# Kernel tuning notes

Measured on AMD Instinct MI355X. Metric: run time of the kernel, lower is better.

The kernel has to match this reference:

```python
import jax, jax.numpy as jnp
import numpy as np

EPS = 1e-5
N, K, CIN, COUT = 100000, 27, 64, 128


def sparse_conv(x, nbr, W):
    # x: [N, C]; nbr: [N, K] with sentinel index N meaning 'no neighbor'
    x_pad = jnp.concatenate([x, jnp.zeros((1, x.shape[1]), x.dtype)], axis=0)  # [N+1, C]
    g = x_pad[nbr]  # gather: [N, K, C]
    return jnp.einsum('nkc,kcd->nd', g, W)  # per-offset GEMM, scatter to output sites


def bn_relu(y, gamma, beta):
    # BatchNorm over active sites (training-mode batch statistics), then ReLU
    mu = y.mean(axis=0)
    var = y.var(axis=0)
    return jax.nn.relu((y - mu) * jax.lax.rsqrt(var + EPS) * gamma + beta)


def setup_inputs() -> dict:
    key = jax.random.key(0)
    ks = jax.random.split(key, 5)
    x = jax.random.normal(ks[0], (N, CIN), dtype=jnp.float32)
    # sentinel N indicates missing neighbor (maps to zero-padded row)
    nbr = jax.random.randint(ks[1], (N, K), 0, N + 1)
    W1 = jax.random.normal(ks[2], (K, CIN, COUT), dtype=jnp.float32) * (1.0 / np.sqrt(K * CIN))
    W2 = jax.random.normal(ks[3], (K, COUT, COUT), dtype=jnp.float32) * (1.0 / np.sqrt(K * COUT))
    W_skip = jax.random.normal(ks[4], (CIN, COUT), dtype=jnp.float32) * (1.0 / np.sqrt(CIN))
    return {
        'x': x, 'nbr': nbr,
        'W1': W1, 'gamma1': jnp.ones((COUT,), jnp.float32), 'beta1': jnp.zeros((COUT,), jnp.float32),
        'W2': W2, 'gamma2': jnp.ones((COUT,), jnp.float32), 'beta2': jnp.zeros((COUT,), jnp.float32),
        'W_skip': W_skip,
    }


def reference(x, nbr, W1, gamma1, beta1, W2, gamma2, beta2, W_skip):
    identity = x @ W_skip                      # 1x1 conv skip (same coords)
    h = bn_relu(sparse_conv(x, nbr, W1), gamma1, beta1)
    h = bn_relu(sparse_conv(h, nbr, W2), gamma2, beta2)
    return h + identity
```

## Files before the change

### kernel.cpp

```cpp
#include <hip/hip_runtime.h>
#include <hip/hip_bf16.h>

#define NSITES 100000
#define KOFFS 27
#define CIN 64
#define COUT 128

typedef unsigned short u16;
typedef __attribute__((ext_vector_type(8))) short s16x8;
typedef __attribute__((ext_vector_type(4))) float f32x4;

static __device__ __forceinline__ u16 f2bf(float f) {
    union { float f; unsigned u; } x; x.f = f;
    return (u16)((x.u + 0x7FFFu + ((x.u >> 16) & 1u)) >> 16);
}
static __device__ __forceinline__ float bf2f(u16 v) {
    union { unsigned u; float f; } x; x.u = ((unsigned)v) << 16;
    return x.f;
}

__global__ void prep_kernel(const float* __restrict__ W1, const float* __restrict__ W2,
                            const float* __restrict__ Wsk,
                            u16* __restrict__ W1t, u16* __restrict__ W2t,
                            u16* __restrict__ Wskt, float* __restrict__ zero_area) {
    int i = blockIdx.x * 256 + threadIdx.x;
    if (i < 27 * 64 * 128) {
        int k = i / 8192, r = i & 8191, d = r >> 6, c = r & 63;
        W1t[i] = f2bf(W1[k * 8192 + c * 128 + d]);
        return;
    }
    i -= 27 * 64 * 128;
    if (i < 27 * 128 * 128) {
        int k = i / 16384, r = i & 16383, d = r >> 7, c = r & 127;
        W2t[i] = f2bf(W2[k * 16384 + c * 128 + d]);
        return;
    }
    i -= 27 * 128 * 128;
    if (i < 8192) {
        int d = i >> 6, c = i & 63;
        Wskt[i] = f2bf(Wsk[c * 128 + d]);
        return;
    }
    i -= 8192;
    zero_area[i] = 0.0f;
}

__global__ void convert_x_kernel(const float* __restrict__ x, u16* __restrict__ xb) {
    long long e = ((long long)blockIdx.x * 256 + threadIdx.x) * 8;
    if (e >= (long long)(NSITES + 1) * CIN) return;
    s16x8 o;
    if (e < (long long)NSITES * CIN) {
        float4 v0 = *(const float4*)(x + e);
        float4 v1 = *(const float4*)(x + e + 4);
        o[0] = (short)f2bf(v0.x); o[1] = (short)f2bf(v0.y);
        o[2] = (short)f2bf(v0.z); o[3] = (short)f2bf(v0.w);
        o[4] = (short)f2bf(v1.x); o[5] = (short)f2bf(v1.y);
        o[6] = (short)f2bf(v1.z); o[7] = (short)f2bf(v1.w);
    } else {
#pragma unroll
        for (int j = 0; j < 8; ++j) o[j] = 0;
    }
    *(s16x8*)(xb + e) = o;
}

template <int CK, bool IDENT_FUSE, bool STATS>
__global__ __launch_bounds__(256, (CK == 64 ? 4 : 3)) void conv_kernel(
    const u16* __restrict__ xin, const int* __restrict__ nbr,
    const u16* __restrict__ Wt, u16* __restrict__ yout,
    float* __restrict__ psum, float* __restrict__ psq, int nk,
    const u16* __restrict__ Wskt, float* __restrict__ outid) {
    constexpr int STRIDE = CK + 8;
    constexpr int KSTEPS = CK / 32;
    constexpr int CPR = CK / 8;
    constexpr int RPP = 256 / CPR;
    constexpr int NPASS = 64 / RPP;
    __shared__ __align__(16) u16 a_tile[2][64 * STRIDE];
    __shared__ int nbr_tile[64 * KOFFS];

    const int tid = threadIdx.x;
    const int wave = tid >> 6;
    const int lane = tid & 63;
    const int m = lane & 15;
    const int q = lane >> 4;
    const int n0 = blockIdx.x * 64;
    const int wc = wave * 32;
    const int srow = tid / CPR;
    const int schunk = tid % CPR;

    for (int i = tid; i < 64 * KOFFS; i += 256) {
        int r = i / KOFFS;
        int kk = i - r * KOFFS;
        int row = n0 + r;
        nbr_tile[i] = (row < NSITES) ? nbr[row * KOFFS + kk] : NSITES;
    }
    __syncthreads();

    f32x4 acc[4][2];
#pragma unroll
    for (int rt = 0; rt < 4; ++rt)
#pragma unroll
        for (int ct = 0; ct < 2; ++ct)
#pragma unroll
            for (int r = 0; r < 4; ++r) acc[rt][ct][r] = 0.0f;

    s16x8 ag[NPASS];
#pragma unroll
    for (int p = 0; p < NPASS; ++p) {
        int r = p * RPP + srow;
        ag[p] = *(const s16x8*)(xin + (long long)nbr_tile[r * KOFFS] * CK + schunk * 8);
    }
#pragma unroll
    for (int p = 0; p < NPASS; ++p)
        *(s16x8*)(a_tile[0] + (p * RPP + srow) * STRIDE + schunk * 8) = ag[p];
    __syncthreads();

    for (int k = 0; k < nk; ++k) {
        const u16* abuf = a_tile[k & 1];
        u16* wbuf = a_tile[(k + 1) & 1];
        const bool more = (k + 1 < nk);

        if (more) {
#pragma unroll
            for (int p = 0; p < NPASS; ++p) {
                int r = p * RPP + srow;
                ag[p] = *(const s16x8*)(xin + (long long)nbr_tile[r * KOFFS + k + 1] * CK + schunk * 8);
            }
        }

        s16x8 bf[2][KSTEPS];
        const u16* wb = Wt + (long long)k * (COUT * CK);
#pragma unroll
        for (int ct = 0; ct < 2; ++ct)
#pragma unroll
            for (int ks = 0; ks < KSTEPS; ++ks)
                bf[ct][ks] = *(const s16x8*)(wb + (wc + ct * 16 + m) * CK + ks * 32 + q * 8);

#pragma unroll
        for (int ks = 0; ks < KSTEPS; ++ks) {
            s16x8 af[4];
#pragma unroll
            for (int rt = 0; rt < 4; ++rt)
                af[rt] = *(const s16x8*)(abuf + (rt * 16 + m) * STRIDE + ks * 32 + q * 8);
#pragma unroll
            for (int rt = 0; rt < 4; ++rt)
#pragma unroll
                for (int ct = 0; ct < 2; ++ct)
                    acc[rt][ct] = __builtin_amdgcn_mfma_f32_16x16x32_bf16(
                        af[rt], bf[ct][ks], acc[rt][ct], 0, 0, 0);
        }

        if (more) {
#pragma unroll
            for (int p = 0; p < NPASS; ++p)
                *(s16x8*)(wbuf + (p * RPP + srow) * STRIDE + schunk * 8) = ag[p];
        }
        __syncthreads();
    }

#pragma unroll
    for (int rt = 0; rt < 4; ++rt) {
        int rowb = n0 + rt * 16 + q * 4;
#pragma unroll
        for (int ct = 0; ct < 2; ++ct) {
            int col = wc + ct * 16 + m;
#pragma unroll
            for (int r = 0; r < 4; ++r) {
                int row = rowb + r;
                if (row < NSITES) yout[(long long)row * COUT + col] = f2bf(acc[rt][ct][r]);
            }
        }
    }

    if (STATS) {
#pragma unroll
        for (int ct = 0; ct < 2; ++ct) {
            float s = 0.f, ss = 0.f;
#pragma unroll
            for (int rt = 0; rt < 4; ++rt)
#pragma unroll
                for (int r = 0; r < 4; ++r) {
                    float v = acc[rt][ct][r];
                    s += v; ss += v * v;
                }
            s += __shfl_xor(s, 16); ss += __shfl_xor(ss, 16);
            s += __shfl_xor(s, 32); ss += __shfl_xor(ss, 32);
            if (q == 0) {
                int col = wc + ct * 16 + m;
                int slot = blockIdx.x & 63;
                atomicAdd(psum + slot * COUT + col, s);
                atomicAdd(psq + slot * COUT + col, ss);
            }
        }
    }

    if (IDENT_FUSE) {
#pragma unroll
        for (int rt = 0; rt < 4; ++rt)
#pragma unroll
            for (int ct = 0; ct < 2; ++ct)
#pragma unroll
                for (int r = 0; r < 4; ++r) acc[rt][ct][r] = 0.0f;
        s16x8 aid[NPASS];
#pragma unroll
        for (int p = 0; p < NPASS; ++p) {
            int row = n0 + p * RPP + srow;
            long long idx = (row < NSITES) ? row : NSITES;
            aid[p] = *(const s16x8*)(xin + idx * CK + schunk * 8);
        }
        s16x8 bfi[2][KSTEPS];
#pragma unroll
        for (int ct = 0; ct < 2; ++ct)
#pragma unroll
            for (int ks = 0; ks < KSTEPS; ++ks)
                bfi[ct][ks] = *(const s16x8*)(Wskt + (wc + ct * 16 + m) * CK + ks * 32 + q * 8);
#pragma unroll
        for (int p = 0; p < NPASS; ++p)
            *(s16x8*)(a_tile[0] + (p * RPP + srow) * STRIDE + schunk * 8) = aid[p];
        __syncthreads();
#pragma unroll
        for (int ks = 0; ks < KSTEPS; ++ks) {
            s16x8 af[4];
#pragma unroll
            for (int rt = 0; rt < 4; ++rt)
                af[rt] = *(const s16x8*)(a_tile[0] + (rt * 16 + m) * STRIDE + ks * 32 + q * 8);
#pragma unroll
            for (int rt = 0; rt < 4; ++rt)
#pragma unroll
                for (int ct = 0; ct < 2; ++ct)
                    acc[rt][ct] = __builtin_amdgcn_mfma_f32_16x16x32_bf16(
                        af[rt], bfi[ct][ks], acc[rt][ct], 0, 0, 0);
        }
#pragma unroll
        for (int rt = 0; rt < 4; ++rt) {
            int rowb = n0 + rt * 16 + q * 4;
#pragma unroll
            for (int ct = 0; ct < 2; ++ct) {
                int col = wc + ct * 16 + m;
#pragma unroll
                for (int r = 0; r < 4; ++r) {
                    int row = rowb + r;
                    if (row < NSITES) outid[(long long)row * COUT + col] = acc[rt][ct][r];
                }
            }
        }
    }
}

__global__ void bn_stats_kernel(const float* __restrict__ psum, const float* __restrict__ psq,
                                const float* __restrict__ gamma, const float* __restrict__ beta,
                                float* __restrict__ ab) {
    int col = threadIdx.x;
    float s = 0.f, ss = 0.f;
    for (int i = 0; i < 64; ++i) { s += psum[i * COUT + col]; ss += psq[i * COUT + col]; }
    const float inv_n = 1.0f / (float)NSITES;
    float mu = s * inv_n;
    float var = ss * inv_n - mu * mu;
    float rs = rsqrtf(var + 1e-5f);
    float a = gamma[col] * rs;
    ab[col] = a;
    ab[COUT + col] = beta[col] - mu * a;
}

__global__ void bn_apply_kernel(const u16* __restrict__ y, const float* __restrict__ ab,
                                u16* __restrict__ h) {
    long long e = ((long long)blockIdx.x * 256 + threadIdx.x) * 8;
    if (e >= (long long)(NSITES + 1) * COUT) return;
    s16x8 o;
    if (e < (long long)NSITES * COUT) {
        int cb = (int)(e & (COUT - 1));
        s16x8 v = *(const s16x8*)(y + e);
#pragma unroll
        for (int j = 0; j < 8; ++j) {
            float r = bf2f((u16)v[j]) * ab[cb + j] + ab[COUT + cb + j];
            o[j] = (short)f2bf(fmaxf(r, 0.f));
        }
    } else {
#pragma unroll
        for (int j = 0; j < 8; ++j) o[j] = 0;
    }
    *(s16x8*)(h + e) = o;
}

__global__ void final_kernel(const u16* __restrict__ y, const float* __restrict__ ab,
                             float* __restrict__ out) {
    long long e = ((long long)blockIdx.x * 256 + threadIdx.x) * 8;
    if (e >= (long long)NSITES * COUT) return;
    int cb = (int)(e & (COUT - 1));
    s16x8 v = *(const s16x8*)(y + e);
    float4 i0 = *(const float4*)(out + e);
    float4 i1 = *(const float4*)(out + e + 4);
    float is[8] = {i0.x, i0.y, i0.z, i0.w, i1.x, i1.y, i1.z, i1.w};
    float os[8];
#pragma unroll
    for (int j = 0; j < 8; ++j) {
        float r = bf2f((u16)v[j]) * ab[cb + j] + ab[COUT + cb + j];
        os[j] = fmaxf(r, 0.f) + is[j];
    }
    *(float4*)(out + e) = make_float4(os[0], os[1], os[2], os[3]);
    *(float4*)(out + e + 4) = make_float4(os[4], os[5], os[6], os[7]);
}

extern "C" void kernel_launch(void* const* d_in, const int* in_sizes, int n_in,
                              void* d_out, int out_size, void* d_ws, size_t ws_size,
                              hipStream_t stream) {
    const float* x   = (const float*)d_in[0];
    const int*   nbr = (const int*)d_in[1];
    const float* W1  = (const float*)d_in[2];
    const float* g1  = (const float*)d_in[3];
    const float* b1  = (const float*)d_in[4];
    const float* W2  = (const float*)d_in[5];
    const float* g2  = (const float*)d_in[6];
    const float* b2  = (const float*)d_in[7];
    const float* Wsk = (const float*)d_in[8];
    float* out = (float*)d_out;

    char* ws = (char*)d_ws;
    u16*   xb   = (u16*)(ws);
    u16*   W1t  = (u16*)(ws + 12800128);
    u16*   W2t  = (u16*)(ws + 13242496);
    u16*   Wskt = (u16*)(ws + 14127232);
    u16*   y    = (u16*)(ws + 14143616);
    u16*   h1   = (u16*)(ws + 39743616);
    float* ps1  = (float*)(ws + 65343872);
    float* pq1  = ps1 + 8192;
    float* ps2  = pq1 + 8192;
    float* pq2  = ps2 + 8192;
    float* ab1  = pq2 + 8192;
    float* ab2  = ab1 + 256;

    const int NBLK = (NSITES + 63) / 64;

    prep_kernel<<<2752, 256, 0, stream>>>(W1, W2, Wsk, W1t, W2t, Wskt, ps1);
    convert_x_kernel<<<3126, 256, 0, stream>>>(x, xb);
    conv_kernel<64, true, true><<<NBLK, 256, 0, stream>>>(xb, nbr, W1t, y, ps1, pq1, KOFFS, Wskt, out);
    bn_stats_kernel<<<1, 128, 0, stream>>>(ps1, pq1, g1, b1, ab1);
    bn_apply_kernel<<<6251, 256, 0, stream>>>(y, ab1, h1);
    conv_kernel<128, false, true><<<NBLK, 256, 0, stream>>>(h1, nbr, W2t, y, ps2, pq2, KOFFS, nullptr, nullptr);
    bn_stats_kernel<<<1, 128, 0, stream>>>(ps2, pq2, g2, b2, ab2);
    final_kernel<<<6250, 256, 0, stream>>>(y, ab2, out);
}
```

Before: 467.9 us.

## Drop neighbor LDS tile, swizzle A-tile LDS layout, prefetch indices in registers

Removes the per-block neighbor-index shared-memory tile and instead has each thread load its own neighbor index one offset ahead into registers, overlapping the index fetch with the gather. The padded A-tile row stride is replaced by an XOR swizzle on 16-byte chunks to avoid LDS bank conflicts while using less LDS. With the smaller LDS footprint, launch bounds now request 4 blocks per CU for both channel widths. The aim is higher occupancy and less LDS traffic, at the cost of a dependent global index load chain per step and extra register pressure for the CK=128 variant.

```diff
diff --git a/kernel.cpp b/kernel.cpp
--- a/kernel.cpp
+++ b/kernel.cpp
@@ -64,18 +64,17 @@
 }
 
 template <int CK, bool IDENT_FUSE, bool STATS>
-__global__ __launch_bounds__(256, (CK == 64 ? 4 : 3)) void conv_kernel(
+__global__ __launch_bounds__(256, 4) void conv_kernel(
     const u16* __restrict__ xin, const int* __restrict__ nbr,
     const u16* __restrict__ Wt, u16* __restrict__ yout,
     float* __restrict__ psum, float* __restrict__ psq, int nk,
     const u16* __restrict__ Wskt, float* __restrict__ outid) {
-    constexpr int STRIDE = CK + 8;
     constexpr int KSTEPS = CK / 32;
     constexpr int CPR = CK / 8;
+    constexpr int SWZ = CPR - 1;
     constexpr int RPP = 256 / CPR;
     constexpr int NPASS = 64 / RPP;
-    __shared__ __align__(16) u16 a_tile[2][64 * STRIDE];
-    __shared__ int nbr_tile[64 * KOFFS];
+    __shared__ __align__(16) u16 a_tile[2][64 * CK];
 
     const int tid = threadIdx.x;
     const int wave = tid >> 6;
@@ -87,14 +86,6 @@
     const int srow = tid / CPR;
     const int schunk = tid % CPR;
 
-    for (int i = tid; i < 64 * KOFFS; i += 256) {
-        int r = i / KOFFS;
-        int kk = i - r * KOFFS;
-        int row = n0 + r;
-        nbr_tile[i] = (row < NSITES) ? nbr[row * KOFFS + kk] : NSITES;
-    }
-    __syncthreads();
-
     f32x4 acc[4][2];
 #pragma unroll
     for (int rt = 0; rt < 4; ++rt)
@@ -103,15 +94,26 @@
 #pragma unroll
             for (int r = 0; r < 4; ++r) acc[rt][ct][r] = 0.0f;
 
+    int nidx[NPASS];
     s16x8 ag[NPASS];
+#pragma unroll
+    for (int p = 0; p < NPASS; ++p) {
+        int row = n0 + p * RPP + srow;
+        nidx[p] = (row < NSITES) ? nbr[row * KOFFS] : NSITES;
+    }
+#pragma unroll
+    for (int p = 0; p < NPASS; ++p)
+        ag[p] = *(const s16x8*)(xin + (long long)nidx[p] * CK + schunk * 8);
+#pragma unroll
+    for (int p = 0; p < NPASS; ++p) {
+        int row = n0 + p * RPP + srow;
+        nidx[p] = (row < NSITES && nk > 1) ? nbr[row * KOFFS + 1] : NSITES;
+    }
 #pragma unroll
     for (int p = 0; p < NPASS; ++p) {
         int r = p * RPP + srow;
-        ag[p] = *(const s16x8*)(xin + (long long)nbr_tile[r * KOFFS] * CK + schunk * 8);
-    }
-#pragma unroll
-    for (int p = 0; p < NPASS; ++p)
-        *(s16x8*)(a_tile[0] + (p * RPP + srow) * STRIDE + schunk * 8) = ag[p];
+        *(s16x8*)(a_tile[0] + r * CK + ((schunk ^ (r & SWZ)) * 8)) = ag[p];
+    }
     __syncthreads();
 
     for (int k = 0; k < nk; ++k) {
@@ -119,14 +121,6 @@
         u16* wbuf = a_tile[(k + 1) & 1];
         const bool more = (k + 1 < nk);
 
-        if (more) {
-#pragma unroll
-            for (int p = 0; p < NPASS; ++p) {
-                int r = p * RPP + srow;
-                ag[p] = *(const s16x8*)(xin + (long long)nbr_tile[r * KOFFS + k + 1] * CK + schunk * 8);
-            }
-        }
-
         s16x8 bf[2][KSTEPS];
         const u16* wb = Wt + (long long)k * (COUT * CK);
 #pragma unroll
@@ -135,12 +129,25 @@
             for (int ks = 0; ks < KSTEPS; ++ks)
                 bf[ct][ks] = *(const s16x8*)(wb + (wc + ct * 16 + m) * CK + ks * 32 + q * 8);
 
+        if (more) {
+#pragma unroll
+            for (int p = 0; p < NPASS; ++p)
+                ag[p] = *(const s16x8*)(xin + (long long)nidx[p] * CK + schunk * 8);
+#pragma unroll
+            for (int p = 0; p < NPASS; ++p) {
+                int row = n0 + p * RPP + srow;
+                nidx[p] = (row < NSITES && k + 2 < nk) ? nbr[row * KOFFS + k + 2] : NSITES;
+            }
+        }
+
 #pragma unroll
         for (int ks = 0; ks < KSTEPS; ++ks) {
             s16x8 af[4];
 #pragma unroll
-            for (int rt = 0; rt < 4; ++rt)
-                af[rt] = *(const s16x8*)(abuf + (rt * 16 + m) * STRIDE + ks * 32 + q * 8);
+            for (int rt = 0; rt < 4; ++rt) {
+                int r = rt * 16 + m;
+                af[rt] = *(const s16x8*)(abuf + r * CK + (((ks * 4 + q) ^ (r & SWZ)) * 8));
+            }
 #pragma unroll
             for (int rt = 0; rt < 4; ++rt)
 #pragma unroll
@@ -151,8 +158,10 @@
 
         if (more) {
 #pragma unroll
-            for (int p = 0; p < NPASS; ++p)
-                *(s16x8*)(wbuf + (p * RPP + srow) * STRIDE + schunk * 8) = ag[p];
+            for (int p = 0; p < NPASS; ++p) {
+                int r = p * RPP + srow;
+                *(s16x8*)(wbuf + r * CK + ((schunk ^ (r & SWZ)) * 8)) = ag[p];
+            }
         }
         __syncthreads();
     }
@@ -214,15 +223,19 @@
             for (int ks = 0; ks < KSTEPS; ++ks)
                 bfi[ct][ks] = *(const s16x8*)(Wskt + (wc + ct * 16 + m) * CK + ks * 32 + q * 8);
 #pragma unroll
-        for (int p = 0; p < NPASS; ++p)
-            *(s16x8*)(a_tile[0] + (p * RPP + srow) * STRIDE + schunk * 8) = aid[p];
+        for (int p = 0; p < NPASS; ++p) {
+            int r = p * RPP + srow;
+            *(s16x8*)(a_tile[0] + r * CK + ((schunk ^ (r & SWZ)) * 8)) = aid[p];
+        }
         __syncthreads();
 #pragma unroll
         for (int ks = 0; ks < KSTEPS; ++ks) {
             s16x8 af[4];
 #pragma unroll
-            for (int rt = 0; rt < 4; ++rt)
-                af[rt] = *(const s16x8*)(a_tile[0] + (rt * 16 + m) * STRIDE + ks * 32 + q * 8);
+            for (int rt = 0; rt < 4; ++rt) {
+                int r = rt * 16 + m;
+                af[rt] = *(const s16x8*)(a_tile[0] + r * CK + (((ks * 4 + q) ^ (r & SWZ)) * 8));
+            }
 #pragma unroll
             for (int rt = 0; rt < 4; ++rt)
 #pragma unroll
```

Result: no change. 467.2 us (-0.2%).
